# Kernel optimization log

Hardware: AMD Instinct MI355X
Metric: run time of the kernel (lower is better)

Reference implementation:

```python
import jax, jax.numpy as jnp
import numpy as np

K = 3          # involution kernel size
GROUPS = 32    # channels == GROUPS * K*K
BN_EPS = 1e-5

def _conv1x1(x, W, b):
    # x: (B,C,H,W), W: (Co,C), b: (Co,)
    return jnp.einsum('bchw,oc->bohw', x, W) + b[None, :, None, None]

def setup_inputs() -> dict:
    key = jax.random.key(0)
    ks = jax.random.split(key, 5)
    C = GROUPS * K * K  # 288
    x = jax.random.normal(ks[0], (8, C, 64, 64), dtype=jnp.float32)
    Wi = jax.random.normal(ks[1], (C, C), dtype=jnp.float32) * 0.05
    bi = jnp.zeros((C,), dtype=jnp.float32)
    gamma = jnp.ones((C,), dtype=jnp.float32)
    beta = jnp.zeros((C,), dtype=jnp.float32)
    Wo = jax.random.normal(ks[2], (C, C), dtype=jnp.float32) * 0.05
    bo = jnp.zeros((C,), dtype=jnp.float32)
    return {"x": x, "Wi": Wi, "bi": bi, "gamma": gamma, "beta": beta, "Wo": Wo, "bo": bo}

def reference(x, Wi, bi, gamma, beta, Wo, bo):
    B, C, H, W = x.shape
    # kernel generation branch (stride=1 -> avgpool is identity)
    tmp = jax.nn.relu(_conv1x1(x, Wi, bi))
    # BatchNorm2d in training mode: batch stats over (N,H,W), biased variance
    mean = jnp.mean(tmp, axis=(0, 2, 3), keepdims=True)
    var = jnp.var(tmp, axis=(0, 2, 3), keepdims=True)
    tmp = (tmp - mean) * jax.lax.rsqrt(var + BN_EPS)
    tmp = tmp * gamma[None, :, None, None] + beta[None, :, None, None]
    ker = _conv1x1(tmp, Wo, bo)                       # (B, G*K^2, H, W)
    ker = ker.reshape(B, GROUPS, K * K, H, W)         # (B, G, K^2, H, W)
    # unfold: extract KxK patches with padding (K-1)//2, stride 1
    p = (K - 1) // 2
    xp = jnp.pad(x, ((0, 0), (0, 0), (p, p), (p, p)))
    patches = jnp.stack(
        [xp[:, :, i:i + H, j:j + W] for i in range(K) for j in range(K)],
        axis=2,
    )  # (B, C, K^2, H, W), kernel-position minor — matches torch unfold layout
    patches = patches.reshape(B, GROUPS, C // GROUPS, K * K, H, W)
    # per-pixel dynamic kernel multiply + sum over kernel positions
    out = jnp.einsum('bgkhw,bgckhw->bgchw', ker, patches)
    return out.reshape(B, C, H, W)
```

## Files before the change

kernel.cpp:

```cpp
#include <hip/hip_runtime.h>

#define CH   288
#define GRPS 32
#define CPG  9
#define IMH  64
#define IMW  64
#define HW   4096
#define NB   8
#define NPX  (NB * HW)
#define BN_EPS 1e-5f

typedef short bf16x8 __attribute__((ext_vector_type(8)));
typedef float f32x4  __attribute__((ext_vector_type(4)));

#define XT_OFF   0u
#define WIB_OFF  18874368u
#define WOS_OFF  19040256u
#define S1_OFF   19206144u
#define S2_OFF   19207296u
#define SC_OFF   19208448u
#define SH_OFF   19209600u
#define BO2_OFF  19210752u

__device__ __forceinline__ unsigned short f2b(float f) {
    unsigned int u = __float_as_uint(f);
    return (unsigned short)((u + 0x7fffu + ((u >> 16) & 1u)) >> 16);
}
__device__ __forceinline__ float b2f(unsigned short h) {
    return __uint_as_float(((unsigned int)h) << 16);
}

#define GLDS(g, l) __builtin_amdgcn_global_load_lds( \
    (const __attribute__((address_space(1))) void*)(g), \
    (__attribute__((address_space(3))) void*)(l), 16, 0, 0)

__device__ __forceinline__ f32x4 mfma16(bf16x8 a, bf16x8 b, f32x4 c) {
    return __builtin_amdgcn_mfma_f32_16x16x32_bf16(a, b, c, 0, 0, 0);
}

#define SUBT 22528

#define TS 40
__global__ __launch_bounds__(256) void k_transpose(const float* __restrict__ x,
                                                   unsigned short* __restrict__ xt) {
    __shared__ unsigned short T[64 * TS];
    const int tid = threadIdx.x;
    const int p0 = blockIdx.x * 64;
    const int c0 = blockIdx.y * 32;
    const int b  = blockIdx.z;
    #pragma unroll
    for (int it = 0; it < 2; ++it) {
        const int item  = it * 256 + tid;
        const int c_loc = item >> 4;
        const int p4    = item & 15;
        const float4 v = *(const float4*)(x + (size_t)(b * CH + c0 + c_loc) * HW + p0 + p4 * 4);
        const int px = p4 * 4;
        T[(px + 0) * TS + c_loc] = f2b(v.x);
        T[(px + 1) * TS + c_loc] = f2b(v.y);
        T[(px + 2) * TS + c_loc] = f2b(v.z);
        T[(px + 3) * TS + c_loc] = f2b(v.w);
    }
    __syncthreads();
    const int px_loc = tid >> 2;
    const int cq     = tid & 3;
    const uint4 o = *(const uint4*)((const char*)T + px_loc * (TS * 2) + cq * 16);
    *(uint4*)(xt + ((size_t)b * HW + p0 + px_loc) * CH + c0 + cq * 8) = o;
}

__global__ __launch_bounds__(256) void k_cvt_wi(const float* __restrict__ Wi,
                                                unsigned short* __restrict__ Wib) {
    const int idx = blockIdx.x * 256 + threadIdx.x;
    const float4 v = ((const float4*)Wi)[idx];
    unsigned short h[4] = {f2b(v.x), f2b(v.y), f2b(v.z), f2b(v.w)};
    *(uint2*)(Wib + (size_t)idx * 4) = *(const uint2*)h;
}

__global__ __launch_bounds__(256) void k_gemm1(const unsigned short* __restrict__ Wib,
                                               const float* __restrict__ bi,
                                               unsigned short* __restrict__ xt,
                                               float* __restrict__ s1g) {
    __shared__ unsigned short smem[3 * 11264];
    char* smc = (char*)smem;

    const int tid  = threadIdx.x;
    const int wave = tid >> 6;
    const int lane = tid & 63;
    const int q    = lane >> 4;
    const int r    = lane & 15;
    const int pxh  = wave & 1;
    const int chh  = wave >> 1;
    const int p0   = blockIdx.x * 64;

    f32x4 acc[2][9];
    #pragma unroll
    for (int t = 0; t < 2; ++t)
        #pragma unroll
        for (int j = 0; j < 9; ++j) acc[t][j] = (f32x4)0.0f;

    const int lrow = lane >> 2;
    const int lp   = lane & 3;

    for (int k0 = 0; k0 < CH; k0 += 96) {
        #pragma unroll
        for (int kk = 0; kk < 3; ++kk) {
            for (int s = wave; s < 22; s += 4) {
                const int row = s * 16 + lrow;
                const int sc  = lp ^ ((row >> 1) & 3);
                const unsigned short* g = (s < 4)
                    ? xt  + (size_t)(p0 + row) * CH + k0 + kk * 32 + sc * 8
                    : Wib + (size_t)(row - 64) * CH + k0 + kk * 32 + sc * 8;
                GLDS(g, smc + kk * SUBT + s * 1024);
            }
        }
        __syncthreads();
        bf16x8 xf[3][2];
        #pragma unroll
        for (int kk = 0; kk < 3; ++kk)
            #pragma unroll
            for (int t = 0; t < 2; ++t) {
                const int row = pxh * 32 + t * 16 + r;
                xf[kk][t] = *(const bf16x8*)(smc + kk * SUBT + row * 64 + ((q ^ ((row >> 1) & 3)) * 16));
            }
        #pragma unroll
        for (int j = 0; j < 9; ++j) {
            const int ro = 64 + chh * 144 + j * 16 + r;
            #pragma unroll
            for (int kk = 0; kk < 3; ++kk) {
                const bf16x8 wf = *(const bf16x8*)(smc + kk * SUBT + ro * 64 + ((q ^ ((ro >> 1) & 3)) * 16));
                acc[0][j] = mfma16(wf, xf[kk][0], acc[0][j]);
                acc[1][j] = mfma16(wf, xf[kk][1], acc[1][j]);
            }
        }
        __syncthreads();
    }

    float* sstat = (float*)(smc + 18432);
    for (int c2 = tid; c2 < 576; c2 += 256) sstat[c2] = 0.0f;
    __syncthreads();

    #pragma unroll 1
    for (int j = 0; j < 9; ++j) {
        const int cb = chh * 144 + j * 16 + q * 4;
        const float4 b4 = *(const float4*)(bi + cb);
        float a1[4] = {0.f, 0.f, 0.f, 0.f}, a2[4] = {0.f, 0.f, 0.f, 0.f};
        #pragma unroll
        for (int t = 0; t < 2; ++t) {
            float v0 = fmaxf(acc[t][j][0] + b4.x, 0.0f);
            float v1 = fmaxf(acc[t][j][1] + b4.y, 0.0f);
            float v2 = fmaxf(acc[t][j][2] + b4.z, 0.0f);
            float v3 = fmaxf(acc[t][j][3] + b4.w, 0.0f);
            a1[0] += v0; a1[1] += v1; a1[2] += v2; a1[3] += v3;
            a2[0] += v0 * v0; a2[1] += v1 * v1; a2[2] += v2 * v2; a2[3] += v3 * v3;
        }
        #pragma unroll
        for (int m = 1; m < 16; m <<= 1) {
            #pragma unroll
            for (int i = 0; i < 4; ++i) {
                a1[i] += __shfl_xor(a1[i], m, 64);
                a2[i] += __shfl_xor(a2[i], m, 64);
            }
        }
        if (r == 0) {
            #pragma unroll
            for (int i = 0; i < 4; ++i) {
                atomicAdd(&sstat[cb + i], a1[i]);
                atomicAdd(&sstat[288 + cb + i], a2[i]);
            }
        }
    }

    #pragma unroll
    for (int ph = 0; ph < 2; ++ph) {
        const int lr = pxh * 16 + r;
        #pragma unroll
        for (int j = 0; j < 9; ++j) {
            const int cb = chh * 144 + j * 16 + q * 4;
            const float4 b4 = *(const float4*)(bi + cb);
            unsigned short h[4];
            h[0] = f2b(fmaxf(acc[ph][j][0] + b4.x, 0.0f));
            h[1] = f2b(fmaxf(acc[ph][j][1] + b4.y, 0.0f));
            h[2] = f2b(fmaxf(acc[ph][j][2] + b4.z, 0.0f));
            h[3] = f2b(fmaxf(acc[ph][j][3] + b4.w, 0.0f));
            *(uint2*)(smc + lr * 576 + cb * 2) = *(const uint2*)h;
        }
        __syncthreads();
        for (int idx = tid; idx < 1152; idx += 256) {
            const int row = idx / 36;
            const int off = idx - row * 36;
            const int gpx = p0 + ph * 16 + row + (row & 16);
            *(uint4*)(xt + (size_t)gpx * CH + off * 8) =
                *(const uint4*)(smc + row * 576 + off * 16);
        }
        if (ph == 0) {
            for (int c2 = tid; c2 < 576; c2 += 256)
                atomicAdd(&s1g[c2], sstat[c2]);
        }
        __syncthreads();
    }
}

__global__ __launch_bounds__(320) void k_scale(const float* __restrict__ s1,
                                               const float* __restrict__ s2,
                                               const float* __restrict__ gamma,
                                               const float* __restrict__ beta,
                                               float* __restrict__ scale,
                                               float* __restrict__ shift) {
    const int c = threadIdx.x;
    if (c < CH) {
        const float inv = 1.0f / (float)(NB * HW);
        const float mean = s1[c] * inv;
        const float var  = s2[c] * inv - mean * mean;
        const float rs   = rsqrtf(var + BN_EPS);
        const float sc   = gamma[c] * rs;
        scale[c] = sc;
        shift[c] = beta[c] - mean * sc;
    }
}

__global__ __launch_bounds__(64) void k_fold(const float* __restrict__ Wo,
                                             const float* __restrict__ bo,
                                             const float* __restrict__ scale,
                                             const float* __restrict__ shift,
                                             unsigned short* __restrict__ Wos,
                                             float* __restrict__ bo2) {
    const int m = blockIdx.x;
    const int t = threadIdx.x;
    float s = 0.0f;
    for (int k = t; k < CH; k += 64) {
        const float wv = Wo[(size_t)m * CH + k];
        s += wv * shift[k];
        Wos[(size_t)m * CH + k] = f2b(wv * scale[k]);
    }
    #pragma unroll
    for (int off = 32; off > 0; off >>= 1) s += __shfl_down(s, off, 64);
    if (t == 0) bo2[m] = bo[m] + s;
}

#define KLS2 68
__global__ __launch_bounds__(256) void k_gemm2_invol(const unsigned short* __restrict__ xt,
                                                     const unsigned short* __restrict__ Wos,
                                                     const float* __restrict__ bo2,
                                                     const float* __restrict__ x,
                                                     float* __restrict__ out) {
    __shared__ unsigned short smem[3 * 11264];
    char* smc = (char*)smem;
    unsigned short* kerL = smem;

    const int tid  = threadIdx.x;
    const int wave = tid >> 6;
    const int lane = tid & 63;
    const int q    = lane >> 4;
    const int r    = lane & 15;
    const int pxh  = wave & 1;
    const int chh  = wave >> 1;
    const int p0   = blockIdx.x * 64;
    const int b    = blockIdx.y;
    const int h    = blockIdx.x;
    const size_t rowbase = (size_t)b * HW + p0;

    f32x4 acc[2][9];
    #pragma unroll
    for (int t = 0; t < 2; ++t)
        #pragma unroll
        for (int j = 0; j < 9; ++j) acc[t][j] = (f32x4)0.0f;

    const int lrow = lane >> 2;
    const int lp   = lane & 3;

    for (int k0 = 0; k0 < CH; k0 += 96) {
        #pragma unroll
        for (int kk = 0; kk < 3; ++kk) {
            for (int s = wave; s < 22; s += 4) {
                const int row = s * 16 + lrow;
                const int sc  = lp ^ ((row >> 1) & 3);
                const unsigned short* g = (s < 18)
                    ? Wos + (size_t)row * CH + k0 + kk * 32 + sc * 8
                    : xt  + (rowbase + row - 288) * CH + k0 + kk * 32 + sc * 8;
                GLDS(g, smc + kk * SUBT + s * 1024);
            }
        }
        __syncthreads();
        bf16x8 xf[3][2];
        #pragma unroll
        for (int kk = 0; kk < 3; ++kk)
            #pragma unroll
            for (int t = 0; t < 2; ++t) {
                const int xr = 288 + pxh * 32 + t * 16 + r;
                xf[kk][t] = *(const bf16x8*)(smc + kk * SUBT + xr * 64 + ((q ^ ((xr >> 1) & 3)) * 16));
            }
        #pragma unroll
        for (int j = 0; j < 9; ++j) {
            const int wr = chh * 144 + j * 16 + r;
            #pragma unroll
            for (int kk = 0; kk < 3; ++kk) {
                const bf16x8 wf = *(const bf16x8*)(smc + kk * SUBT + wr * 64 + ((q ^ ((wr >> 1) & 3)) * 16));
                acc[0][j] = mfma16(wf, xf[kk][0], acc[0][j]);
                acc[1][j] = mfma16(wf, xf[kk][1], acc[1][j]);
            }
        }
        __syncthreads();
    }

    #pragma unroll
    for (int j = 0; j < 9; ++j) {
        const int cb = chh * 144 + j * 16 + q * 4;
        const float4 bz = *(const float4*)(bo2 + cb);
        #pragma unroll
        for (int t = 0; t < 2; ++t) {
            const int pxl = pxh * 32 + t * 16 + r;
            kerL[(cb + 0) * KLS2 + pxl] = f2b(acc[t][j][0] + bz.x);
            kerL[(cb + 1) * KLS2 + pxl] = f2b(acc[t][j][1] + bz.y);
            kerL[(cb + 2) * KLS2 + pxl] = f2b(acc[t][j][2] + bz.z);
            kerL[(cb + 3) * KLS2 + pxl] = f2b(acc[t][j][3] + bz.w);
        }
    }
    __syncthreads();

    const int tm = tid >> 4;
    const int tn = tid & 15;
    const int wb = tn * 4;
    #pragma unroll 1
    for (int i = 0; i < 18; ++i) {
        const int ch = tm + 16 * i;
        const int cb = (ch / CPG) * CPG;
        float xv[3][6];
        #pragma unroll
        for (int dr = 0; dr < 3; ++dr) {
            const int hh = h + dr - 1;
            const bool rv = (hh >= 0) && (hh < IMH);
            const float* xr2 = x + ((size_t)(b * CH + ch) * IMH + (rv ? hh : 0)) * IMW;
            if (rv) {
                const float4 m4 = *(const float4*)(xr2 + wb);
                xv[dr][1] = m4.x; xv[dr][2] = m4.y; xv[dr][3] = m4.z; xv[dr][4] = m4.w;
                xv[dr][0] = (wb > 0)       ? xr2[wb - 1] : 0.0f;
                xv[dr][5] = (wb + 4 < IMW) ? xr2[wb + 4] : 0.0f;
            } else {
                #pragma unroll
                for (int j = 0; j < 6; ++j) xv[dr][j] = 0.0f;
            }
        }
        float o[4] = {0.0f, 0.0f, 0.0f, 0.0f};
        #pragma unroll
        for (int k = 0; k < 9; ++k) {
            const int dr = k / 3, dc = k % 3;
            const uint2 kk = *(const uint2*)(kerL + (cb + k) * KLS2 + tn * 4);
            const unsigned short* ks = (const unsigned short*)&kk;
            #pragma unroll
            for (int j = 0; j < 4; ++j)
                o[j] += b2f(ks[j]) * xv[dr][j + dc];
        }
        float4 ov = {o[0], o[1], o[2], o[3]};
        *(float4*)(out + ((size_t)(b * CH + ch) * IMH + h) * IMW + wb) = ov;
    }
}

extern "C" void kernel_launch(void* const* d_in, const int* in_sizes, int n_in,
                              void* d_out, int out_size, void* d_ws, size_t ws_size,
                              hipStream_t stream) {
    const float* x     = (const float*)d_in[0];
    const float* Wi    = (const float*)d_in[1];
    const float* bi    = (const float*)d_in[2];
    const float* gamma = (const float*)d_in[3];
    const float* beta  = (const float*)d_in[4];
    const float* Wo    = (const float*)d_in[5];
    const float* bo    = (const float*)d_in[6];
    float* out = (float*)d_out;

    char* ws = (char*)d_ws;
    unsigned short* xt  = (unsigned short*)(ws + XT_OFF);
    unsigned short* Wib = (unsigned short*)(ws + WIB_OFF);
    unsigned short* Wos = (unsigned short*)(ws + WOS_OFF);
    float* s1    = (float*)(ws + S1_OFF);
    float* s2    = (float*)(ws + S2_OFF);
    float* scale = (float*)(ws + SC_OFF);
    float* shift = (float*)(ws + SH_OFF);
    float* bo2   = (float*)(ws + BO2_OFF);

    k_transpose<<<dim3(HW / 64, CH / 32, NB), 256, 0, stream>>>(x, xt);
    k_cvt_wi<<<dim3(CH * CH / 1024), 256, 0, stream>>>(Wi, Wib);
    hipMemsetAsync(ws + S1_OFF, 0, 2 * CH * sizeof(float), stream);
    k_gemm1<<<dim3(NPX / 64), 256, 0, stream>>>(Wib, bi, xt, s1);
    k_scale<<<dim3(1), 320, 0, stream>>>(s1, s2, gamma, beta, scale, shift);
    k_fold<<<dim3(CH), 64, 0, stream>>>(Wo, bo, scale, shift, Wos, bo2);
    k_gemm2_invol<<<dim3(HW / 64, NB), 256, 0, stream>>>(xt, Wos, bo2, x, out);
}
```

Measured before the change: 191.4 us.

## Stage full activation tile once and double-buffer weight K-slices in both GEMMs

Both GEMM kernels now load the whole 64-pixel by 288-channel activation tile into LDS up front. Weight K-slices of 32 are streamed through a two-buffer ring, using explicit vmcnt waits and raw barriers so the next slice loads while the current one computes. Before, the kernel did three rounds of synchronous 96-wide K chunks with full syncthreads. The change aims to overlap global-to-LDS traffic with MFMA work, at the cost of more barriers per K step and a larger LDS footprint (72 KB), which may lower occupancy.

```diff
diff --git a/kernel.cpp b/kernel.cpp
--- a/kernel.cpp
+++ b/kernel.cpp
@@ -22,6 +22,9 @@
 #define SH_OFF   19209600u
 #define BO2_OFF  19210752u
 
+#define XB 36864
+#define WB 18432
+
 __device__ __forceinline__ unsigned short f2b(float f) {
     unsigned int u = __float_as_uint(f);
     return (unsigned short)((u + 0x7fffu + ((u >> 16) & 1u)) >> 16);
@@ -37,8 +40,6 @@
 __device__ __forceinline__ f32x4 mfma16(bf16x8 a, bf16x8 b, f32x4 c) {
     return __builtin_amdgcn_mfma_f32_16x16x32_bf16(a, b, c, 0, 0, 0);
 }
-
-#define SUBT 22528
 
 #define TS 40
 __global__ __launch_bounds__(256) void k_transpose(const float* __restrict__ x,
@@ -75,12 +76,49 @@
     *(uint2*)(Wib + (size_t)idx * 4) = *(const uint2*)h;
 }
 
+#define GEMM_STEP(KK, WBASE) do {                                              \
+    bf16x8 xf0, xf1;                                                           \
+    { const int row0 = pxh * 32 + r;                                           \
+      xf0 = *(const bf16x8*)(smc + row0 * 576 + (KK) * 64 +                    \
+                             ((q ^ ((row0 >> 1) & 3)) * 16)); }                \
+    { const int row1 = pxh * 32 + 16 + r;                                      \
+      xf1 = *(const bf16x8*)(smc + row1 * 576 + (KK) * 64 +                    \
+                             ((q ^ ((row1 >> 1) & 3)) * 16)); }                \
+    _Pragma("unroll")                                                          \
+    for (int j = 0; j < 9; ++j) {                                              \
+        const int ro = chh * 144 + j * 16 + r;                                 \
+        const bf16x8 wf = *(const bf16x8*)((WBASE) + ro * 64 +                 \
+                             ((q ^ ((ro >> 1) & 3)) * 16));                    \
+        acc[0][j] = mfma16(wf, xf0, acc[0][j]);                                \
+        acc[1][j] = mfma16(wf, xf1, acc[1][j]);                                \
+    }                                                                          \
+} while (0)
+
+#define STAGE_W(WSRC, K0v, WDST) do {                                          \
+    for (int s = wave; s < 18; s += 4) {                                       \
+        const int row = s * 16 + lrow;                                         \
+        const int sc  = lp ^ ((row >> 1) & 3);                                 \
+        GLDS((WSRC) + (size_t)row * CH + (K0v) + sc * 8, (WDST) + s * 1024);   \
+    }                                                                          \
+} while (0)
+
+#define STAGE_X(XSRC) do {                                                     \
+    for (int s = wave; s < 36; s += 4) {                                       \
+        const int d   = s * 1024 + lane * 16;                                  \
+        const int px  = d / 576;                                               \
+        const int rem = d - px * 576;                                          \
+        const int kc  = rem >> 6;                                              \
+        const int ch  = (rem >> 4) & 3;                                        \
+        const int sc  = ch ^ ((px >> 1) & 3);                                  \
+        GLDS((XSRC) + (size_t)px * CH + kc * 32 + sc * 8, smc + s * 1024);     \
+    }                                                                          \
+} while (0)
+
 __global__ __launch_bounds__(256) void k_gemm1(const unsigned short* __restrict__ Wib,
                                                const float* __restrict__ bi,
                                                unsigned short* __restrict__ xt,
                                                float* __restrict__ s1g) {
-    __shared__ unsigned short smem[3 * 11264];
-    char* smc = (char*)smem;
+    __shared__ char smc[XB + 2 * WB];
 
     const int tid  = threadIdx.x;
     const int wave = tid >> 6;
@@ -90,49 +128,34 @@
     const int pxh  = wave & 1;
     const int chh  = wave >> 1;
     const int p0   = blockIdx.x * 64;
-
-    f32x4 acc[2][9];
-    #pragma unroll
-    for (int t = 0; t < 2; ++t)
-        #pragma unroll
-        for (int j = 0; j < 9; ++j) acc[t][j] = (f32x4)0.0f;
-
     const int lrow = lane >> 2;
     const int lp   = lane & 3;
 
-    for (int k0 = 0; k0 < CH; k0 += 96) {
-        #pragma unroll
-        for (int kk = 0; kk < 3; ++kk) {
-            for (int s = wave; s < 22; s += 4) {
-                const int row = s * 16 + lrow;
-                const int sc  = lp ^ ((row >> 1) & 3);
-                const unsigned short* g = (s < 4)
-                    ? xt  + (size_t)(p0 + row) * CH + k0 + kk * 32 + sc * 8
-                    : Wib + (size_t)(row - 64) * CH + k0 + kk * 32 + sc * 8;
-                GLDS(g, smc + kk * SUBT + s * 1024);
-            }
-        }
-        __syncthreads();
-        bf16x8 xf[3][2];
-        #pragma unroll
-        for (int kk = 0; kk < 3; ++kk)
-            #pragma unroll
-            for (int t = 0; t < 2; ++t) {
-                const int row = pxh * 32 + t * 16 + r;
-                xf[kk][t] = *(const bf16x8*)(smc + kk * SUBT + row * 64 + ((q ^ ((row >> 1) & 3)) * 16));
-            }
-        #pragma unroll
-        for (int j = 0; j < 9; ++j) {
-            const int ro = 64 + chh * 144 + j * 16 + r;
-            #pragma unroll
-            for (int kk = 0; kk < 3; ++kk) {
-                const bf16x8 wf = *(const bf16x8*)(smc + kk * SUBT + ro * 64 + ((q ^ ((ro >> 1) & 3)) * 16));
-                acc[0][j] = mfma16(wf, xf[kk][0], acc[0][j]);
-                acc[1][j] = mfma16(wf, xf[kk][1], acc[1][j]);
-            }
-        }
-        __syncthreads();
-    }
+    f32x4 acc[2][9];
+    #pragma unroll
+    for (int t = 0; t < 2; ++t)
+        #pragma unroll
+        for (int j = 0; j < 9; ++j) acc[t][j] = (f32x4)0.0f;
+
+    STAGE_X(xt + (size_t)p0 * CH);
+    STAGE_W(Wib, 0, smc + XB);
+    asm volatile("s_waitcnt vmcnt(0)" ::: "memory");
+    __builtin_amdgcn_s_barrier();
+
+    #pragma unroll 1
+    for (int kk = 0; kk < 8; ++kk) {
+        char* wnext = smc + XB + ((kk + 1) & 1) * WB;
+        STAGE_W(Wib, (kk + 1) * 32, wnext);
+        asm volatile("s_waitcnt vmcnt(4)" ::: "memory");
+        __builtin_amdgcn_s_barrier();
+        char* wcur = smc + XB + (kk & 1) * WB;
+        GEMM_STEP(kk, wcur);
+        __builtin_amdgcn_s_barrier();
+    }
+    asm volatile("s_waitcnt vmcnt(0)" ::: "memory");
+    __builtin_amdgcn_s_barrier();
+    GEMM_STEP(8, smc + XB);
+    __syncthreads();
 
     float* sstat = (float*)(smc + 18432);
     for (int c2 = tid; c2 < 576; c2 += 256) sstat[c2] = 0.0f;
@@ -242,9 +265,8 @@
                                                      const float* __restrict__ bo2,
                                                      const float* __restrict__ x,
                                                      float* __restrict__ out) {
-    __shared__ unsigned short smem[3 * 11264];
-    char* smc = (char*)smem;
-    unsigned short* kerL = smem;
+    __shared__ char smc[XB + 2 * WB];
+    unsigned short* kerL = (unsigned short*)smc;
 
     const int tid  = threadIdx.x;
     const int wave = tid >> 6;
@@ -257,49 +279,34 @@
     const int b    = blockIdx.y;
     const int h    = blockIdx.x;
     const size_t rowbase = (size_t)b * HW + p0;
-
-    f32x4 acc[2][9];
-    #pragma unroll
-    for (int t = 0; t < 2; ++t)
-        #pragma unroll
-        for (int j = 0; j < 9; ++j) acc[t][j] = (f32x4)0.0f;
-
     const int lrow = lane >> 2;
     const int lp   = lane & 3;
 
-    for (int k0 = 0; k0 < CH; k0 += 96) {
-        #pragma unroll
-        for (int kk = 0; kk < 3; ++kk) {
-            for (int s = wave; s < 22; s += 4) {
-                const int row = s * 16 + lrow;
-                const int sc  = lp ^ ((row >> 1) & 3);
-                const unsigned short* g = (s < 18)
-                    ? Wos + (size_t)row * CH + k0 + kk * 32 + sc * 8
-                    : xt  + (rowbase + row - 288) * CH + k0 + kk * 32 + sc * 8;
-                GLDS(g, smc + kk * SUBT + s * 1024);
-            }
-        }
-        __syncthreads();
-        bf16x8 xf[3][2];
-        #pragma unroll
-        for (int kk = 0; kk < 3; ++kk)
-            #pragma unroll
-            for (int t = 0; t < 2; ++t) {
-                const int xr = 288 + pxh * 32 + t * 16 + r;
-                xf[kk][t] = *(const bf16x8*)(smc + kk * SUBT + xr * 64 + ((q ^ ((xr >> 1) & 3)) * 16));
-            }
-        #pragma unroll
-        for (int j = 0; j < 9; ++j) {
-            const int wr = chh * 144 + j * 16 + r;
-            #pragma unroll
-            for (int kk = 0; kk < 3; ++kk) {
-                const bf16x8 wf = *(const bf16x8*)(smc + kk * SUBT + wr * 64 + ((q ^ ((wr >> 1) & 3)) * 16));
-                acc[0][j] = mfma16(wf, xf[kk][0], acc[0][j]);
-                acc[1][j] = mfma16(wf, xf[kk][1], acc[1][j]);
-            }
-        }
-        __syncthreads();
-    }
+    f32x4 acc[2][9];
+    #pragma unroll
+    for (int t = 0; t < 2; ++t)
+        #pragma unroll
+        for (int j = 0; j < 9; ++j) acc[t][j] = (f32x4)0.0f;
+
+    STAGE_X(xt + rowbase * CH);
+    STAGE_W(Wos, 0, smc + XB);
+    asm volatile("s_waitcnt vmcnt(0)" ::: "memory");
+    __builtin_amdgcn_s_barrier();
+
+    #pragma unroll 1
+    for (int kk = 0; kk < 8; ++kk) {
+        char* wnext = smc + XB + ((kk + 1) & 1) * WB;
+        STAGE_W(Wos, (kk + 1) * 32, wnext);
+        asm volatile("s_waitcnt vmcnt(4)" ::: "memory");
+        __builtin_amdgcn_s_barrier();
+        char* wcur = smc + XB + (kk & 1) * WB;
+        GEMM_STEP(kk, wcur);
+        __builtin_amdgcn_s_barrier();
+    }
+    asm volatile("s_waitcnt vmcnt(0)" ::: "memory");
+    __builtin_amdgcn_s_barrier();
+    GEMM_STEP(8, smc + XB);
+    __syncthreads();
 
     #pragma unroll
     for (int j = 0; j < 9; ++j) {
```

Result: faster. 186.5 us (-2.6%).
